# Kernel optimization log

Hardware: AMD Instinct MI355X
Metric: run time of the kernel (lower is better)

## Reference

```python
import jax, jax.numpy as jnp
import numpy as np

DIM, QK, GS, DEPTH, VOCAB, ROT = 16, 128, 256, 8, 1024, 32
EPS = 1e-5


def scale_norm(x, g):
    # ScaleNorm: x / max(||x|| * dim^-0.5, eps) * g
    norm = jnp.linalg.norm(x, axis=-1, keepdims=True) * (DIM ** -0.5)
    return x / jnp.clip(norm, EPS) * g


def rotate_half(x):
    # interleaved pairs: (x0,x1,x2,x3,...) -> (-x1,x0,-x3,x2,...)
    xr = x.reshape(x.shape[:-1] + (-1, 2))
    a, b = xr[..., 0], xr[..., 1]
    return jnp.stack((-b, a), axis=-1).reshape(x.shape)


def apply_rotary(x, cos, sin):
    # rotary applied to first ROT dims only
    xr, xp = x[..., :ROT], x[..., ROT:]
    return jnp.concatenate([xr * cos + rotate_half(xr) * sin, xp], axis=-1)


def flash_layer(x, p, cos, sin, keymask, n):
    b = x.shape[0]
    normed = scale_norm(x, p['norm_g'])
    # shift_tokens: first half of channels shifted forward by one position
    xs, xp = jnp.split(normed, 2, axis=-1)
    xs = jnp.pad(xs, ((0, 0), (1, 0), (0, 0)))[:, :-1]
    normed = jnp.concatenate([xs, xp], axis=-1)
    hid = jax.nn.silu(normed @ p['Wh'] + p['bh'])  # [b,n,64]
    v, gate = jnp.split(hid, 2, axis=-1)           # each [b,n,32]
    qk = jax.nn.silu(normed @ p['Wqk'] + p['bqk'])  # [b,n,128]
    offs = qk[..., None, :] * p['gamma'] + p['beta']  # [b,n,4,128]
    quad_q, lin_q, quad_k, lin_k = [apply_rotary(offs[..., i, :], cos, sin) for i in range(4)]
    pad = (-n) % GS
    grp = lambda t: jnp.pad(t, ((0, 0), (0, pad), (0, 0))).reshape(b, -1, GS, t.shape[-1])
    quad_q, quad_k, lin_q, lin_k, vg = map(grp, (quad_q, quad_k, lin_q, lin_k, v))
    # quadratic (local, within-group) attention with ReLU^2
    sim = jnp.einsum('bgid,bgjd->bgij', quad_q, quad_k) / GS
    attn = jnp.square(jax.nn.relu(sim)) * keymask  # mask out padded keys
    quad_out = jnp.einsum('bgij,bgjd->bgid', attn, vg)
    # linear (global, across-group) attention, reduced over groups
    lin_kv = jnp.einsum('bgnd,bgne->bde', lin_k, vg) / n
    lin_out = jnp.einsum('bgnd,bde->bgne', lin_q, lin_kv)
    out = (quad_out + lin_out).reshape(b, -1, v.shape[-1])[:, :n]
    out = gate * out
    return out @ p['Wo'] + p['bo'] + x


def forward(kmer_data, token_emb, pos_scale, norm_g, Wh, bh, Wqk, bqk, gamma, beta, Wo, bo, final_g, Wl, bl, W1, b1, W2, b2):
    b, n = kmer_data.shape
    x = token_emb[kmer_data]  # [b,n,16]
    t = jnp.arange(n, dtype=jnp.float32)
    # ScaledSinuEmbedding
    inv = 1.0 / (10000.0 ** (jnp.arange(0, DIM, 2, dtype=jnp.float32) / DIM))
    sinu = t[:, None] * inv[None, :]
    pos = jnp.concatenate([jnp.sin(sinu), jnp.cos(sinu)], axis=-1) * pos_scale
    x = x + pos
    # rotary tables (dim 32, interleaved repeat)
    rinv = 1.0 / (10000.0 ** (jnp.arange(0, ROT, 2, dtype=jnp.float32) / ROT))
    rf = jnp.repeat(t[:, None] * rinv[None, :], 2, axis=-1)  # [n,32]
    cos, sin = jnp.cos(rf), jnp.sin(rf)
    # key mask for padded positions (996 -> 1024)
    pad = (-n) % GS
    keymask = jnp.pad(jnp.ones((n,), jnp.float32), (0, pad)).reshape(1, -1, 1, GS)
    for i in range(DEPTH):
        p = dict(norm_g=norm_g[i], Wh=Wh[i], bh=bh[i], Wqk=Wqk[i], bqk=bqk[i],
                 gamma=gamma[i], beta=beta[i], Wo=Wo[i], bo=bo[i])
        x = flash_layer(x, p, cos, sin, keymask, n)
    logits = scale_norm(x, final_g) @ Wl + bl  # [b,n,1024]
    h = jnp.max(logits, axis=-1)               # AdaptiveMaxPool1d(1) + Flatten -> [b,n]
    h = jax.nn.relu(h @ W1 + b1)
    return h @ W2 + b2                          # [b,1]


def setup_inputs() -> dict:
    key = jax.random.key(0)
    ks = jax.random.split(key, 12)
    r = lambda k, shape, s: jax.random.normal(k, shape, jnp.float32) * s
    return {
        'kmer_data': jax.random.randint(ks[0], (128, 996), 0, VOCAB),
        'token_emb': r(ks[1], (VOCAB, DIM), 1.0),
        'pos_scale': jnp.float32(1.0),
        'norm_g': jnp.ones((DEPTH,), jnp.float32),
        'Wh': r(ks[2], (DEPTH, DIM, 64), 0.1),
        'bh': jnp.zeros((DEPTH, 64), jnp.float32),
        'Wqk': r(ks[3], (DEPTH, DIM, QK), 0.1),
        'bqk': jnp.zeros((DEPTH, QK), jnp.float32),
        'gamma': 1.0 + r(ks[4], (DEPTH, 4, QK), 0.02),
        'beta': r(ks[5], (DEPTH, 4, QK), 0.02),
        'Wo': r(ks[6], (DEPTH, 32, DIM), 0.1),
        'bo': jnp.zeros((DEPTH, DIM), jnp.float32),
        'final_g': jnp.float32(1.0),
        'Wl': r(ks[7], (DIM, VOCAB), 0.1),
        'bl': jnp.zeros((VOCAB,), jnp.float32),
        'W1': r(ks[8], (996, 32), 0.05),
        'b1': jnp.zeros((32,), jnp.float32),
        'W2': r(ks[9], (32, 1), 0.1),
        'b2': jnp.zeros((1,), jnp.float32),
    }


def reference(kmer_data, token_emb, pos_scale, norm_g, Wh, bh, Wqk, bqk, gamma, beta, Wo, bo, final_g, Wl, bl, W1, b1, W2, b2):
    return forward(kmer_data, token_emb, pos_scale, norm_g, Wh, bh, Wqk, bqk,
                   gamma, beta, Wo, bo, final_g, Wl, bl, W1, b1, W2, b2)
```

## Files before the change

kernel.cpp:

```cpp
#include <hip/hip_runtime.h>

typedef short s16x8 __attribute__((ext_vector_type(8)));
typedef float f32x4 __attribute__((ext_vector_type(4)));

#define NB    128
#define NTOK  996
#define NPAD  1024
#define NGRP  4
#define GSZ   256
#define NLAY  8

__device__ __forceinline__ float bf2f(unsigned short u){
    unsigned int v = ((unsigned int)u) << 16;
    return __uint_as_float(v);
}
__device__ __forceinline__ unsigned short f2bf(float f){
    unsigned int x = __float_as_uint(f);
    unsigned int r = (x + 0x7fffu + ((x >> 16) & 1u)) >> 16;
    return (unsigned short)r;
}
__device__ __forceinline__ unsigned int packbf(float a, float b){
    return (unsigned int)f2bf(a) | ((unsigned int)f2bf(b) << 16);
}
__device__ __forceinline__ float silu(float v){
    return v / (1.0f + __expf(-v));
}

__device__ __forceinline__ void bar_lds(){
    asm volatile("s_waitcnt lgkmcnt(0)\n\ts_barrier" ::: "memory");
}

__device__ __forceinline__ s16x8 derive_core(const unsigned short* __restrict__ qrow, int d0,
        float4 g0, float4 g1, float4 b0, float4 b1,
        const float* __restrict__ rp, bool rot){
    uint4 u = *(const uint4*)(qrow + d0);
    float y0 = bf2f((unsigned short)(u.x & 0xffffu))*g0.x + b0.x;
    float y1 = bf2f((unsigned short)(u.x >> 16))    *g0.y + b0.y;
    float y2 = bf2f((unsigned short)(u.y & 0xffffu))*g0.z + b0.z;
    float y3 = bf2f((unsigned short)(u.y >> 16))    *g0.w + b0.w;
    float y4 = bf2f((unsigned short)(u.z & 0xffffu))*g1.x + b1.x;
    float y5 = bf2f((unsigned short)(u.z >> 16))    *g1.y + b1.y;
    float y6 = bf2f((unsigned short)(u.w & 0xffffu))*g1.z + b1.z;
    float y7 = bf2f((unsigned short)(u.w >> 16))    *g1.w + b1.w;
    if (rot){
        float4 c4 = *(const float4*)(rp);
        float4 s4 = *(const float4*)(rp + 16);
        float a;
        a = y0; y0 = a*c4.x - y1*s4.x; y1 = y1*c4.x + a*s4.x;
        a = y2; y2 = a*c4.y - y3*s4.y; y3 = y3*c4.y + a*s4.y;
        a = y4; y4 = a*c4.z - y5*s4.z; y5 = y5*c4.z + a*s4.z;
        a = y6; y6 = a*c4.w - y7*s4.w; y7 = y7*c4.w + a*s4.w;
    }
    union { unsigned int uu[4]; s16x8 s; } r;
    r.uu[0] = packbf(y0, y1);
    r.uu[1] = packbf(y2, y3);
    r.uu[2] = packbf(y4, y5);
    r.uu[3] = packbf(y6, y7);
    return r.s;
}

__global__ __launch_bounds__(256) void k_embed(const int* __restrict__ kmer,
                                               const float* __restrict__ emb,
                                               const float* __restrict__ ps,
                                               float* __restrict__ x,
                                               float* __restrict__ rope){
    int gid = blockIdx.x * 256 + threadIdx.x;
    if (gid < NPAD){
        float tf2 = (float)gid;
        #pragma unroll
        for (int i = 0; i < 16; i++){
            float inv = expf(((float)(2*i) / 32.0f) * -9.210340371976184f);
            float ang = tf2 * inv;
            rope[gid*32 + i]      = cosf(ang);
            rope[gid*32 + 16 + i] = sinf(ang);
        }
    }
    if (gid >= NB * NTOK) return;
    int b = gid / NTOK;
    int tt = gid - b * NTOK;
    int idx = kmer[gid];
    const float* er = emb + (size_t)idx * 16;
    float pscale = ps[0];
    float tf = (float)tt;
    float* xr = x + (size_t)gid * 16;
    #pragma unroll
    for (int i = 0; i < 8; i++){
        float inv = expf(((float)(2*i) / 16.0f) * -9.210340371976184f);
        float ang = tf * inv;
        xr[i]     = er[i]     + sinf(ang) * pscale;
        xr[8 + i] = er[8 + i] + cosf(ang) * pscale;
    }
}

__global__ __launch_bounds__(512, 2) void k_pre(const float* __restrict__ x,
                                             const float* __restrict__ Wh, const float* __restrict__ bh,
                                             const float* __restrict__ Wqk, const float* __restrict__ bqk,
                                             const float* __restrict__ norm_g,
                                             const float* __restrict__ gamma, const float* __restrict__ beta,
                                             const float* __restrict__ rope, int layer,
                                             unsigned short* __restrict__ qk,
                                             unsigned short* __restrict__ vT,
                                             unsigned short* __restrict__ gateb,
                                             float* __restrict__ linkvp){
    __shared__ __align__(16) unsigned char sm[58880];
    unsigned short* WcT = (unsigned short*)sm;
    unsigned short* As  = (unsigned short*)(sm + 15360);
    unsigned short* LkT = (unsigned short*)(sm + 15360);
    unsigned short* Vt  = (unsigned short*)(sm + 50176);
    int tid = threadIdx.x;
    int qt = blockIdx.x & 3, b = blockIdx.x >> 2;
    const float* Whl = Wh  + (size_t)layer * 1024;
    const float* Wql = Wqk + (size_t)layer * 2048;
    const float* gLin = gamma + (size_t)layer * 512 + 384;
    const float* bLin = beta  + (size_t)layer * 512 + 384;
    for (int i = tid; i < 1024; i += 512){ int d = i >> 6, c2 = i & 63;  WcT[c2*40 + d] = f2bf(Whl[i]); }
    for (int i = tid; i < 2048; i += 512){ int d = i >> 7, c2 = i & 127; WcT[(64 + c2)*40 + d] = f2bf(Wql[i]); }
    if (tid < 192){
        int i = tid;
        float bv = (i < 64) ? bh[layer*64 + i] : bqk[layer*128 + (i - 64)];
        WcT[i*40 + 16] = f2bf(bv);
        WcT[i*40 + 17] = 0;
        unsigned int* zz = (unsigned int*)(WcT + i*40 + 18);
        #pragma unroll
        for (int k = 0; k < 7; k++) zz[k] = 0u;
    }
    float g = norm_g[layer];
    if (tid < 256){
        int tt = qt*256 + tid;
        int tsafe = tt < NTOK ? tt : (NTOK - 1);
        unsigned int* dd = (unsigned int*)(As + tid * 40);
        const float4* xr4 = (const float4*)(x + ((size_t)b*NTOK + tsafe) * 16);
        float cur[16];
        float s2 = 0.f;
        #pragma unroll
        for (int c2 = 0; c2 < 4; c2++){
            float4 v4 = xr4[c2];
            cur[4*c2] = v4.x; cur[4*c2+1] = v4.y; cur[4*c2+2] = v4.z; cur[4*c2+3] = v4.w;
        }
        #pragma unroll
        for (int d = 0; d < 16; d++) s2 += cur[d]*cur[d];
        float sc = g / fmaxf(sqrtf(s2) * 0.25f, 1e-5f);
        #pragma unroll
        for (int i = 0; i < 4; i++) dd[4 + i] = packbf(cur[8 + 2*i]*sc, cur[9 + 2*i]*sc);
        dd[8] = 0x00003f80u;
        #pragma unroll
        for (int i = 9; i < 16; i++) dd[i] = 0u;
        if (tid < 255){
            unsigned int* ddn = (unsigned int*)(As + (tid+1) * 40);
            #pragma unroll
            for (int i = 0; i < 4; i++) ddn[i] = packbf(cur[2*i]*sc, cur[2*i+1]*sc);
        }
        if (tid == 0){
            if (tt == 0){
                dd[0] = 0u; dd[1] = 0u; dd[2] = 0u; dd[3] = 0u;
            } else {
                const float4* xp4 = (const float4*)(x + ((size_t)b*NTOK + tt - 1) * 16);
                float prv[16]; float p2 = 0.f;
                #pragma unroll
                for (int c2 = 0; c2 < 4; c2++){
                    float4 v4 = xp4[c2];
                    prv[4*c2] = v4.x; prv[4*c2+1] = v4.y; prv[4*c2+2] = v4.z; prv[4*c2+3] = v4.w;
                }
                #pragma unroll
                for (int d = 0; d < 16; d++) p2 += prv[d]*prv[d];
                float sp = g / fmaxf(sqrtf(p2) * 0.25f, 1e-5f);
                #pragma unroll
                for (int i = 0; i < 4; i++) dd[i] = packbf(prv[2*i]*sp, prv[2*i+1]*sp);
            }
        }
    }
    bar_lds();
    int w = tid >> 6, lane = tid & 63, m16 = lane & 15, quad = lane >> 4;
    s16x8 bfr[2];
    #pragma unroll
    for (int nt = 0; nt < 2; nt++)
        bfr[nt] = *(const s16x8*)(As + (w*32 + nt*16 + m16)*40 + quad*8);
    bar_lds();
    f32x4 zacc = {0.f,0.f,0.f,0.f};
    f32x4 lacc[2] = {{0,0,0,0},{0,0,0,0}};
    unsigned int vpk[2][2][2];
    int c = w*16 + m16;
    #pragma unroll
    for (int nt = 0; nt < 2; nt++){
        int ttk = qt*256 + w*32 + nt*16 + m16;
        bool tv = ttk < NTOK;
        size_t rowq = (size_t)b*NPAD + ttk;
        #pragma unroll
        for (int mi = 0; mi < 12; mi++){
            s16x8 wfm = *(const s16x8*)(WcT + (mi*16 + m16)*40 + quad*8);
            f32x4 r = __builtin_amdgcn_mfma_f32_16x16x32_bf16(wfm, bfr[nt], zacc, 0, 0, 0);
            float sv[4];
            #pragma unroll
            for (int reg = 0; reg < 4; reg++) sv[reg] = silu(r[reg]);
            int wc0 = mi*16 + quad*4;
            if (mi < 2){
                unsigned short p0 = tv ? f2bf(sv[0]) : (unsigned short)0;
                unsigned short p1 = tv ? f2bf(sv[1]) : (unsigned short)0;
                unsigned short p2 = tv ? f2bf(sv[2]) : (unsigned short)0;
                unsigned short p3 = tv ? f2bf(sv[3]) : (unsigned short)0;
                Vt[(wc0+0)*136 + c] = p0;
                Vt[(wc0+1)*136 + c] = p1;
                Vt[(wc0+2)*136 + c] = p2;
                Vt[(wc0+3)*136 + c] = p3;
                vpk[nt][mi][0] = (unsigned int)p0 | ((unsigned int)p1 << 16);
                vpk[nt][mi][1] = (unsigned int)p2 | ((unsigned int)p3 << 16);
            } else if (mi < 4){
                *(uint2*)(gateb + rowq*32 + (wc0 - 32)) = make_uint2(packbf(sv[0],sv[1]), packbf(sv[2],sv[3]));
            } else {
                int qd = wc0 - 64;
                *(uint2*)(qk + rowq*128 + qd) = make_uint2(packbf(sv[0],sv[1]), packbf(sv[2],sv[3]));
                float y0 = sv[0]*gLin[qd]   + bLin[qd];
                float y1 = sv[1]*gLin[qd+1] + bLin[qd+1];
                float y2 = sv[2]*gLin[qd+2] + bLin[qd+2];
                float y3 = sv[3]*gLin[qd+3] + bLin[qd+3];
                if (qd < 32){
                    const float* rp = rope + ttk*32 + (qd >> 1);
                    float c0 = rp[0], s0 = rp[16], c1 = rp[1], s1 = rp[17];
                    float a;
                    a = y0; y0 = a*c0 - y1*s0; y1 = y1*c0 + a*s0;
                    a = y2; y2 = a*c1 - y3*s1; y3 = y3*c1 + a*s1;
                }
                LkT[(qd+0)*136 + c] = f2bf(y0);
                LkT[(qd+1)*136 + c] = f2bf(y1);
                LkT[(qd+2)*136 + c] = f2bf(y2);
                LkT[(qd+3)*136 + c] = f2bf(y3);
            }
        }
        bar_lds();
        #pragma unroll
        for (int ks2 = 0; ks2 < 4; ks2++){
            s16x8 a  = *(const s16x8*)(LkT + (w*16 + m16)*136 + ks2*32 + quad*8);
            s16x8 b0 = *(const s16x8*)(Vt + (m16)*136 + ks2*32 + quad*8);
            s16x8 b1 = *(const s16x8*)(Vt + (16 + m16)*136 + ks2*32 + quad*8);
            lacc[0] = __builtin_amdgcn_mfma_f32_16x16x32_bf16(a, b0, lacc[0], 0,0,0);
            lacc[1] = __builtin_amdgcn_mfma_f32_16x16x32_bf16(a, b1, lacc[1], 0,0,0);
        }
        bar_lds();
    }
    {
        unsigned short* mv = (unsigned short*)sm + w*1280;
        #pragma unroll
        for (int nt = 0; nt < 2; nt++){
            #pragma unroll
            for (int mi = 0; mi < 2; mi++){
                int e0 = mi*16 + quad*4;
                mv[(e0+0)*40 + nt*16 + m16] = (unsigned short)(vpk[nt][mi][0] & 0xffffu);
                mv[(e0+1)*40 + nt*16 + m16] = (unsigned short)(vpk[nt][mi][0] >> 16);
                mv[(e0+2)*40 + nt*16 + m16] = (unsigned short)(vpk[nt][mi][1] & 0xffffu);
                mv[(e0+3)*40 + nt*16 + m16] = (unsigned short)(vpk[nt][mi][1] >> 16);
            }
        }
        #pragma unroll
        for (int r2 = 0; r2 < 2; r2++){
            int e = r2*16 + (lane >> 2);
            int cc = (lane & 3) * 8;
            s16x8 vv = *(const s16x8*)(mv + e*40 + cc);
            *(s16x8*)(vT + ((size_t)b*32 + e)*NPAD + qt*256 + w*32 + cc) = vv;
        }
    }
    {
        float* ml = (float*)(sm + 20480) + w*512;
        const float invn = 1.0f / 996.0f;
        #pragma unroll
        for (int j = 0; j < 2; j++)
            #pragma unroll
            for (int reg = 0; reg < 4; reg++)
                ml[(j*16 + m16)*16 + quad*4 + reg] = lacc[j][reg] * invn;
        #pragma unroll
        for (int r2 = 0; r2 < 2; r2++){
            int e = r2*16 + (lane >> 2);
            int dc = (lane & 3) * 4;
            float4 vv = *(const float4*)(ml + e*16 + dc);
            *(float4*)(linkvp + (((size_t)qt*NB + b)*32 + e)*128 + w*16 + dc) = vv;
        }
    }
}

#define KD_SH   8704
#define KD2_BYTES (2*64*136*2)
#define PW_BYTES  (8*32*40*2)
__global__ __launch_bounds__(512, 2) void k_quad(const unsigned short* __restrict__ qk,
                                              const unsigned short* __restrict__ vT,
                                              const unsigned short* __restrict__ gateb,
                                              const float* __restrict__ linkvp,
                                              const float* __restrict__ rope,
                                              const float* __restrict__ gamma, const float* __restrict__ beta,
                                              int layer,
                                              const float* __restrict__ Wo, const float* __restrict__ bo,
                                              float* __restrict__ x){
    __shared__ __align__(16) unsigned char smem[KD2_BYTES + PW_BYTES];
    __shared__ float sWo[512];
    __shared__ float sbo[16];
    unsigned short* Kd   = (unsigned short*)smem;
    unsigned short* Pw   = (unsigned short*)(smem + KD2_BYTES);
    unsigned short* LkBs = (unsigned short*)(smem + KD2_BYTES);
    int tid = threadIdx.x;
    int blk = blockIdx.x;
    int g = blk & 3, b = blk >> 2;
    int tg0 = g * GSZ;
    const float* gamL = gamma + (size_t)layer * 512;
    const float* betL = beta  + (size_t)layer * 512;
    sWo[tid] = Wo[layer*512 + tid];
    if (tid < 16) sbo[tid] = bo[layer*16 + tid];

    int w = tid >> 6, lane = tid & 63, m16 = lane & 15, quad = lane >> 4;

    int kr = tid >> 3, seg = (tid & 7) * 16;
    uint4 pku0, pku1;
    float4 prc0, prc1, prs0, prs1;
    auto LOADK = [&](int ch){
        int tk = tg0 + ch*64 + kr;
        const unsigned short* krow = qk + ((size_t)b*NPAD + tk)*128 + seg;
        pku0 = ((const uint4*)krow)[0];
        pku1 = ((const uint4*)krow)[1];
        if (seg < 32){
            const float* rpk = rope + tk*32 + (seg >> 1);
            prc0 = *(const float4*)(rpk);
            prs0 = *(const float4*)(rpk + 16);
            prc1 = *(const float4*)(rpk + 4);
            prs1 = *(const float4*)(rpk + 20);
        }
    };
    const float* gK = gamL + 256;
    const float* bK = betL + 256;
    auto DERIVEK = [&](uint4& kd0, uint4& kd1){
        #pragma unroll
        for (int h = 0; h < 2; h++){
            uint4 u = h ? pku1 : pku0;
            unsigned int uu[4] = {u.x, u.y, u.z, u.w};
            float y[8];
            #pragma unroll
            for (int k = 0; k < 4; k++){
                int d = h*8 + 2*k;
                y[2*k]   = bf2f((unsigned short)(uu[k] & 0xffffu)) * gK[seg + d]     + bK[seg + d];
                y[2*k+1] = bf2f((unsigned short)(uu[k] >> 16))     * gK[seg + d + 1] + bK[seg + d + 1];
            }
            if (seg < 32){
                float cc[4], ss[4];
                if (h){ cc[0]=prc1.x; cc[1]=prc1.y; cc[2]=prc1.z; cc[3]=prc1.w;
                        ss[0]=prs1.x; ss[1]=prs1.y; ss[2]=prs1.z; ss[3]=prs1.w; }
                else  { cc[0]=prc0.x; cc[1]=prc0.y; cc[2]=prc0.z; cc[3]=prc0.w;
                        ss[0]=prs0.x; ss[1]=prs0.y; ss[2]=prs0.z; ss[3]=prs0.w; }
                #pragma unroll
                for (int p2 = 0; p2 < 4; p2++){
                    float a = y[2*p2], d2 = y[2*p2+1];
                    y[2*p2]   = a*cc[p2] - d2*ss[p2];
                    y[2*p2+1] = d2*cc[p2] + a*ss[p2];
                }
            }
            uint4 kk = make_uint4(packbf(y[0],y[1]), packbf(y[2],y[3]),
                                  packbf(y[4],y[5]), packbf(y[6],y[7]));
            if (h) kd1 = kk; else kd0 = kk;
        }
    };
    auto LOADV = [&](int ch, s16x8 vf[2][2]){
        #pragma unroll
        for (int ks2 = 0; ks2 < 2; ks2++){
            vf[ks2][0] = *(const s16x8*)(vT + ((size_t)b*32 + m16)*NPAD + tg0 + ch*64 + ks2*32 + quad*8);
            vf[ks2][1] = *(const s16x8*)(vT + ((size_t)b*32 + 16 + m16)*NPAD + tg0 + ch*64 + ks2*32 + quad*8);
        }
    };

    LOADK(0);

    int tqA = tg0 + w*32 + m16;
    int tqB = tqA + 16;
    const unsigned short* qrowA = qk + ((size_t)b*NPAD + tqA)*128;
    const unsigned short* qrowB = qk + ((size_t)b*NPAD + tqB)*128;
    const float* rpA = rope + tqA*32 + quad*4;
    const float* rpB = rope + tqB*32 + quad*4;
    s16x8 qf[2][4];
    #pragma unroll
    for (int ks = 0; ks < 4; ks++){
        int d0 = ks*32 + quad*8;
        float4 g0 = *(const float4*)(gamL + d0), g1 = *(const float4*)(gamL + d0 + 4);
        float4 b0 = *(const float4*)(betL + d0), b1 = *(const float4*)(betL + d0 + 4);
        bool rot = (ks == 0) && (quad < 4);
        qf[0][ks] = derive_core(qrowA, d0, g0,g1,b0,b1, rpA, rot);
        qf[1][ks] = derive_core(qrowB, d0, g0,g1,b0,b1, rpB, rot);
    }

    {
        uint4 kd0, kd1;
        DERIVEK(kd0, kd1);
        *(uint4*)(Kd + kr*136 + seg)     = kd0;
        *(uint4*)(Kd + kr*136 + seg + 8) = kd1;
    }
    LOADK(1);
    s16x8 vfA[2][2];
    LOADV(0, vfA);

    f32x4 oacc[2][2] = {{{0,0,0,0},{0,0,0,0}},{{0,0,0,0},{0,0,0,0}}};
    unsigned short* myP = Pw + w*1280;

    #pragma unroll
    for (int ch = 0; ch < 4; ch++){
        bar_lds();
        s16x8 vfB[2][2];
        if (ch < 3) LOADV(ch + 1, vfB);
        unsigned short* Kc = Kd + (ch & 1)*KD_SH;
        #pragma unroll
        for (int np = 0; np < 2; np++){
            f32x4 s00 = {0,0,0,0}, s01 = {0,0,0,0}, s10 = {0,0,0,0}, s11 = {0,0,0,0};
            #pragma unroll
            for (int ks = 0; ks < 4; ks++){
                s16x8 kf0 = *(const s16x8*)(Kc + ((np*2  )*16 + m16)*136 + ks*32 + quad*8);
                s16x8 kf1 = *(const s16x8*)(Kc + ((np*2+1)*16 + m16)*136 + ks*32 + quad*8);
                s00 = __builtin_amdgcn_mfma_f32_16x16x32_bf16(qf[0][ks], kf0, s00, 0,0,0);
                s01 = __builtin_amdgcn_mfma_f32_16x16x32_bf16(qf[0][ks], kf1, s01, 0,0,0);
                s10 = __builtin_amdgcn_mfma_f32_16x16x32_bf16(qf[1][ks], kf0, s10, 0,0,0);
                s11 = __builtin_amdgcn_mfma_f32_16x16x32_bf16(qf[1][ks], kf1, s11, 0,0,0);
            }
            #pragma unroll
            for (int j = 0; j < 2; j++){
                int kl = j*16 + m16;
                bool kv = (tg0 + ch*64 + np*32 + kl) < NTOK;
                #pragma unroll
                for (int reg = 0; reg < 4; reg++){
                    float a0 = fmaxf(j ? s01[reg] : s00[reg], 0.0f);
                    float a1 = fmaxf(j ? s11[reg] : s10[reg], 0.0f);
                    a0 = a0 * a0;
                    a1 = a1 * a1;
                    myP[(quad*4 + reg)*40 + kl]      = kv ? f2bf(a0) : (unsigned short)0;
                    myP[(16 + quad*4 + reg)*40 + kl] = kv ? f2bf(a1) : (unsigned short)0;
                }
            }
            #pragma unroll
            for (int i = 0; i < 2; i++){
                s16x8 pa = *(const s16x8*)(myP + (i*16 + m16)*40 + quad*8);
                oacc[i][0] = __builtin_amdgcn_mfma_f32_16x16x32_bf16(pa, vfA[np][0], oacc[i][0], 0,0,0);
                oacc[i][1] = __builtin_amdgcn_mfma_f32_16x16x32_bf16(pa, vfA[np][1], oacc[i][1], 0,0,0);
            }
            if (np == 0 && ch < 3){
                uint4 kd0, kd1;
                DERIVEK(kd0, kd1);
                unsigned short* Kn = Kd + ((ch+1) & 1)*KD_SH;
                *(uint4*)(Kn + kr*136 + seg)     = kd0;
                *(uint4*)(Kn + kr*136 + seg + 8) = kd1;
                if (ch < 2) LOADK(ch + 2);
            }
        }
        if (ch < 3){
            #pragma unroll
            for (int ks2 = 0; ks2 < 2; ks2++){
                vfA[ks2][0] = vfB[ks2][0];
                vfA[ks2][1] = vfB[ks2][1];
            }
        }
    }
    const float qsc = 1.0f / 65536.0f;
    #pragma unroll
    for (int i = 0; i < 2; i++)
        #pragma unroll
        for (int j = 0; j < 2; j++)
            oacc[i][j] = oacc[i][j] * qsc;
    int e = tid >> 4, dbase = (tid & 15) * 8;
    float4 lp[4][2];
    #pragma unroll
    for (int part = 0; part < 4; part++){
        const float* src = linkvp + (((size_t)part*NB + b)*32 + e)*128 + dbase;
        lp[part][0] = *(const float4*)src;
        lp[part][1] = *(const float4*)(src + 4);
    }
    bar_lds();
    {
        float s[8];
        #pragma unroll
        for (int k = 0; k < 8; k++) s[k] = 0.f;
        #pragma unroll
        for (int part = 0; part < 4; part++){
            s[0]+=lp[part][0].x; s[1]+=lp[part][0].y; s[2]+=lp[part][0].z; s[3]+=lp[part][0].w;
            s[4]+=lp[part][1].x; s[5]+=lp[part][1].y; s[6]+=lp[part][1].z; s[7]+=lp[part][1].w;
        }
        unsigned int* dst = (unsigned int*)(LkBs + e*136 + dbase);
        #pragma unroll
        for (int k = 0; k < 4; k++) dst[k] = packbf(s[2*k], s[2*k+1]);
    }
    bar_lds();
    int pr = lane >> 1, dp2 = (lane & 1) * 8;
    int p = tg0 + w*32 + pr;
    bool pvld = p < NTOK;
    int psafe = pvld ? p : (NTOK - 1);
    const unsigned short* gr = gateb + ((size_t)b*NPAD + psafe)*32;
    uint4 egu[4];
    #pragma unroll
    for (int eh = 0; eh < 4; eh++) egu[eh] = *(const uint4*)(gr + eh*8);
    float* xr = x + ((size_t)b*NTOK + psafe)*16 + dp2;
    float4 ex0 = *(const float4*)xr;
    float4 ex1 = *(const float4*)(xr + 4);
    {
        const float* gamQ = gamL + 128;
        const float* betQ = betL + 128;
        #pragma unroll
        for (int ks = 0; ks < 4; ks++){
            int d0 = ks*32 + quad*8;
            float4 g0 = *(const float4*)(gamQ + d0), g1 = *(const float4*)(gamQ + d0 + 4);
            float4 b0 = *(const float4*)(betQ + d0), b1 = *(const float4*)(betQ + d0 + 4);
            bool rot = (ks == 0) && (quad < 4);
            s16x8 lf0 = derive_core(qrowA, d0, g0,g1,b0,b1, rpA, rot);
            s16x8 lf1 = derive_core(qrowB, d0, g0,g1,b0,b1, rpB, rot);
            #pragma unroll
            for (int j = 0; j < 2; j++){
                s16x8 lb = *(const s16x8*)(LkBs + (j*16 + m16)*136 + ks*32 + quad*8);
                oacc[0][j] = __builtin_amdgcn_mfma_f32_16x16x32_bf16(lf0, lb, oacc[0][j], 0,0,0);
                oacc[1][j] = __builtin_amdgcn_mfma_f32_16x16x32_bf16(lf1, lb, oacc[1][j], 0,0,0);
            }
        }
    }
    float* Obw = (float*)smem + w*1056;
    #pragma unroll
    for (int i = 0; i < 2; i++)
        #pragma unroll
        for (int j = 0; j < 2; j++)
            #pragma unroll
            for (int reg = 0; reg < 4; reg++)
                Obw[(i*16 + quad*4 + reg)*33 + j*16 + m16] = oacc[i][j][reg];
    if (pvld){
        float a[8] = { sbo[dp2]+ex0.x, sbo[dp2+1]+ex0.y, sbo[dp2+2]+ex0.z, sbo[dp2+3]+ex0.w,
                       sbo[dp2+4]+ex1.x, sbo[dp2+5]+ex1.y, sbo[dp2+6]+ex1.z, sbo[dp2+7]+ex1.w };
        #pragma unroll
        for (int eh = 0; eh < 4; eh++){
            unsigned int gg[4] = {egu[eh].x, egu[eh].y, egu[eh].z, egu[eh].w};
            #pragma unroll
            for (int k = 0; k < 4; k++){
                float gv0 = bf2f((unsigned short)(gg[k] & 0xffffu));
                float gv1 = bf2f((unsigned short)(gg[k] >> 16));
                int ee = eh*8 + 2*k;
                float ov0 = Obw[pr*33 + ee] * gv0;
                float ov1 = Obw[pr*33 + ee + 1] * gv1;
                const float* wr0 = &sWo[ee*16 + dp2];
                const float* wr1 = &sWo[(ee+1)*16 + dp2];
                #pragma unroll
                for (int kk = 0; kk < 8; kk++) a[kk] += ov0 * wr0[kk] + ov1 * wr1[kk];
            }
        }
        *(float4*)xr = make_float4(a[0],a[1],a[2],a[3]);
        *(float4*)(xr+4) = make_float4(a[4],a[5],a[6],a[7]);
    }
}

__global__ __launch_bounds__(256) void k_head(const float* __restrict__ x,
                                              const float* __restrict__ Wl, const float* __restrict__ bl,
                                              const float* __restrict__ fg, float* __restrict__ h){
    __shared__ __align__(16) unsigned short WlT[512 * 40];
    __shared__ __align__(16) unsigned short As[256 * 40];
    int tid = threadIdx.x;
    int gid0 = blockIdx.x * 256;
    {
        int t = gid0 + tid;
        const float4* xr4 = (const float4*)(x + (size_t)t * 16);
        float cur[16]; float s2 = 0.f;
        #pragma unroll
        for (int c = 0; c < 4; c++){
            float4 v4 = xr4[c];
            cur[4*c] = v4.x; cur[4*c+1] = v4.y; cur[4*c+2] = v4.z; cur[4*c+3] = v4.w;
        }
        #pragma unroll
        for (int d = 0; d < 16; d++) s2 += cur[d]*cur[d];
        float sc = fg[0] / fmaxf(sqrtf(s2) * 0.25f, 1e-5f);
        unsigned int* dd = (unsigned int*)(As + tid * 40);
        #pragma unroll
        for (int i = 0; i < 8; i++) dd[i] = packbf(cur[2*i]*sc, cur[2*i+1]*sc);
        dd[8] = 0x00003f80u;
        #pragma unroll
        for (int i = 9; i < 16; i++) dd[i] = 0u;
    }
    int w = tid >> 6, lane = tid & 63, m16 = lane & 15, quad = lane >> 4;
    f32x4 vm[4];
    #pragma unroll
    for (int i = 0; i < 4; i++) vm[i] = (f32x4){-3e38f,-3e38f,-3e38f,-3e38f};
    for (int half = 0; half < 2; half++){
        __syncthreads();
        for (int i = tid; i < 8192; i += 256){
            int d = i >> 9, c = i & 511;
            WlT[c*40 + d] = f2bf(Wl[(size_t)d*1024 + half*512 + c]);
        }
        for (int i = tid; i < 512; i += 256){
            WlT[i*40 + 16] = f2bf(bl[half*512 + i]);
            WlT[i*40 + 17] = 0;
            unsigned int* zz = (unsigned int*)(WlT + i*40 + 18);
            #pragma unroll
            for (int k = 0; k < 7; k++) zz[k] = 0u;
        }
        __syncthreads();
        s16x8 af[4];
        #pragma unroll
        for (int i = 0; i < 4; i++)
            af[i] = *(const s16x8*)(As + (w*64 + i*16 + m16)*40 + quad*8);
        f32x4 zacc = {0,0,0,0};
        for (int nt = 0; nt < 32; nt++){
            s16x8 bf = *(const s16x8*)(WlT + (nt*16 + m16)*40 + quad*8);
            #pragma unroll
            for (int i = 0; i < 4; i++){
                f32x4 r = __builtin_amdgcn_mfma_f32_16x16x32_bf16(af[i], bf, zacc, 0,0,0);
                #pragma unroll
                for (int reg = 0; reg < 4; reg++)
                    vm[i][reg] = fmaxf(vm[i][reg], r[reg]);
            }
        }
    }
    #pragma unroll
    for (int i = 0; i < 4; i++){
        #pragma unroll
        for (int off = 1; off < 16; off <<= 1){
            #pragma unroll
            for (int reg = 0; reg < 4; reg++)
                vm[i][reg] = fmaxf(vm[i][reg], __shfl_xor(vm[i][reg], off, 64));
        }
    }
    if (m16 == 0){
        #pragma unroll
        for (int i = 0; i < 4; i++){
            int t0 = gid0 + w*64 + i*16 + quad*4;
            #pragma unroll
            for (int reg = 0; reg < 4; reg++)
                h[t0 + reg] = vm[i][reg];
        }
    }
}

__global__ __launch_bounds__(256) void k_final(const float* __restrict__ h,
                                               const float* __restrict__ W1, const float* __restrict__ b1,
                                               const float* __restrict__ W2, const float* __restrict__ b2,
                                               float* __restrict__ out){
    int b = blockIdx.x;
    int tid = threadIdx.x;
    int j = tid & 31, part = tid >> 5;
    float acc = 0.f;
    for (int i = part; i < NTOK; i += 8)
        acc += h[(size_t)b*NTOK + i] * W1[(size_t)i*32 + j];
    __shared__ float red[8][33];
    red[part][j] = acc;
    __syncthreads();
    if (tid < 32){
        float s = b1[tid];
        #pragma unroll
        for (int p = 0; p < 8; p++) s += red[p][tid];
        s = fmaxf(s, 0.f);
        red[0][tid] = s * W2[tid];
    }
    __syncthreads();
    if (tid == 0){
        float s = b2[0];
        #pragma unroll
        for (int jj = 0; jj < 32; jj++) s += red[0][jj];
        out[b] = s;
    }
}

extern "C" void kernel_launch(void* const* d_in, const int* in_sizes, int n_in,
                              void* d_out, int out_size, void* d_ws, size_t ws_size,
                              hipStream_t stream){
    const int*   kmer  = (const int*)d_in[0];
    const float* emb   = (const float*)d_in[1];
    const float* ps    = (const float*)d_in[2];
    const float* ng    = (const float*)d_in[3];
    const float* Wh    = (const float*)d_in[4];
    const float* bh    = (const float*)d_in[5];
    const float* Wqk   = (const float*)d_in[6];
    const float* bqk   = (const float*)d_in[7];
    const float* gamma = (const float*)d_in[8];
    const float* beta  = (const float*)d_in[9];
    const float* Wo    = (const float*)d_in[10];
    const float* bo    = (const float*)d_in[11];
    const float* fg    = (const float*)d_in[12];
    const float* Wl    = (const float*)d_in[13];
    const float* bl    = (const float*)d_in[14];
    const float* W1    = (const float*)d_in[15];
    const float* b1    = (const float*)d_in[16];
    const float* W2    = (const float*)d_in[17];
    const float* b2    = (const float*)d_in[18];
    float* out = (float*)d_out;

    char* wsp = (char*)d_ws;
    float* x = (float*)wsp;                     wsp += (size_t)NB*NTOK*16*4;
    unsigned short* qk = (unsigned short*)wsp;  wsp += (size_t)NB*NPAD*128*2;
    unsigned short* vT = (unsigned short*)wsp;  wsp += (size_t)NB*32*NPAD*2;
    unsigned short* gateb = (unsigned short*)wsp; wsp += (size_t)NB*NPAD*32*2;
    float* linkvp = (float*)wsp;                wsp += (size_t)4*NB*32*128*4;
    float* rope = (float*)wsp;                  wsp += (size_t)NPAD*32*4;
    float* h = (float*)wsp;                     wsp += (size_t)NB*NTOK*4;

    k_embed<<<(NB*NTOK + 255)/256, 256, 0, stream>>>(kmer, emb, ps, x, rope);
    for (int layer = 0; layer < NLAY; layer++){
        k_pre<<<NB*4, 512, 0, stream>>>(x, Wh, bh, Wqk, bqk, ng, gamma, beta, rope, layer, qk, vT, gateb, linkvp);
        k_quad<<<NB*NGRP, 512, 0, stream>>>(qk, vT, gateb, linkvp, rope, gamma, beta, layer, Wo, bo, x);
    }
    k_head<<<NB*NTOK/256, 256, 0, stream>>>(x, Wl, bl, fg, h);
    k_final<<<NB, 256, 0, stream>>>(h, W1, b1, W2, b2, out);
}
```

Before: 758.3 us.

## Split quad-attention blocks into query halves with smaller key chunks

k_quad now launches two 256-thread blocks per (batch, group), each owning 128 query rows instead of 256. Keys are streamed in 32-row chunks over 8 iterations, and V fragments are loaded directly each chunk rather than software-prefetched. The aim is higher occupancy (launch bounds 256x5) and finer scheduling granularity. In exchange, each half-block re-derives the full group's K tiles and re-reduces the linear-attention KV partials, which duplicates that work, and the loop has more barriers.

Measured after the change: 1.965 ms. 159% more time.

```diff
diff --git a/kernel.cpp b/kernel.cpp
--- a/kernel.cpp
+++ b/kernel.cpp
@@ -276,10 +276,11 @@
     }
 }
 
-#define KD_SH   8704
-#define KD2_BYTES (2*64*136*2)
-#define PW_BYTES  (8*32*40*2)
-__global__ __launch_bounds__(512, 2) void k_quad(const unsigned short* __restrict__ qk,
+#define KQ_CH   32
+#define KD_SH2  (32*136)
+#define KD2B    (2*KD_SH2*2)
+#define PWB     (4*32*40*2)
+__global__ __launch_bounds__(256, 5) void k_quad(const unsigned short* __restrict__ qk,
                                               const unsigned short* __restrict__ vT,
                                               const unsigned short* __restrict__ gateb,
                                               const float* __restrict__ linkvp,
@@ -288,19 +289,21 @@
                                               int layer,
                                               const float* __restrict__ Wo, const float* __restrict__ bo,
                                               float* __restrict__ x){
-    __shared__ __align__(16) unsigned char smem[KD2_BYTES + PW_BYTES];
+    __shared__ __align__(16) unsigned char smem[KD2B + PWB];
     __shared__ float sWo[512];
     __shared__ float sbo[16];
     unsigned short* Kd   = (unsigned short*)smem;
-    unsigned short* Pw   = (unsigned short*)(smem + KD2_BYTES);
-    unsigned short* LkBs = (unsigned short*)(smem + KD2_BYTES);
+    unsigned short* Pw   = (unsigned short*)(smem + KD2B);
+    unsigned short* LkBs = Pw;
     int tid = threadIdx.x;
     int blk = blockIdx.x;
-    int g = blk & 3, b = blk >> 2;
+    int half = blk & 1, g = (blk >> 1) & 3, b = blk >> 3;
     int tg0 = g * GSZ;
+    int qb0 = tg0 + half*128;
     const float* gamL = gamma + (size_t)layer * 512;
     const float* betL = beta  + (size_t)layer * 512;
-    sWo[tid] = Wo[layer*512 + tid];
+    sWo[tid]       = Wo[layer*512 + tid];
+    sWo[tid + 256] = Wo[layer*512 + 256 + tid];
     if (tid < 16) sbo[tid] = bo[layer*16 + tid];
 
     int w = tid >> 6, lane = tid & 63, m16 = lane & 15, quad = lane >> 4;
@@ -309,7 +312,7 @@
     uint4 pku0, pku1;
     float4 prc0, prc1, prs0, prs1;
     auto LOADK = [&](int ch){
-        int tk = tg0 + ch*64 + kr;
+        int tk = tg0 + ch*KQ_CH + kr;
         const unsigned short* krow = qk + ((size_t)b*NPAD + tk)*128 + seg;
         pku0 = ((const uint4*)krow)[0];
         pku1 = ((const uint4*)krow)[1];
@@ -353,17 +356,10 @@
             if (h) kd1 = kk; else kd0 = kk;
         }
     };
-    auto LOADV = [&](int ch, s16x8 vf[2][2]){
-        #pragma unroll
-        for (int ks2 = 0; ks2 < 2; ks2++){
-            vf[ks2][0] = *(const s16x8*)(vT + ((size_t)b*32 + m16)*NPAD + tg0 + ch*64 + ks2*32 + quad*8);
-            vf[ks2][1] = *(const s16x8*)(vT + ((size_t)b*32 + 16 + m16)*NPAD + tg0 + ch*64 + ks2*32 + quad*8);
-        }
-    };
 
     LOADK(0);
 
-    int tqA = tg0 + w*32 + m16;
+    int tqA = qb0 + w*32 + m16;
     int tqB = tqA + 16;
     const unsigned short* qrowA = qk + ((size_t)b*NPAD + tqA)*128;
     const unsigned short* qrowB = qk + ((size_t)b*NPAD + tqB)*128;
@@ -387,65 +383,53 @@
         *(uint4*)(Kd + kr*136 + seg + 8) = kd1;
     }
     LOADK(1);
-    s16x8 vfA[2][2];
-    LOADV(0, vfA);
 
     f32x4 oacc[2][2] = {{{0,0,0,0},{0,0,0,0}},{{0,0,0,0},{0,0,0,0}}};
     unsigned short* myP = Pw + w*1280;
 
-    #pragma unroll
-    for (int ch = 0; ch < 4; ch++){
+    #pragma unroll 2
+    for (int ch = 0; ch < 8; ch++){
         bar_lds();
-        s16x8 vfB[2][2];
-        if (ch < 3) LOADV(ch + 1, vfB);
-        unsigned short* Kc = Kd + (ch & 1)*KD_SH;
-        #pragma unroll
-        for (int np = 0; np < 2; np++){
-            f32x4 s00 = {0,0,0,0}, s01 = {0,0,0,0}, s10 = {0,0,0,0}, s11 = {0,0,0,0};
-            #pragma unroll
-            for (int ks = 0; ks < 4; ks++){
-                s16x8 kf0 = *(const s16x8*)(Kc + ((np*2  )*16 + m16)*136 + ks*32 + quad*8);
-                s16x8 kf1 = *(const s16x8*)(Kc + ((np*2+1)*16 + m16)*136 + ks*32 + quad*8);
-                s00 = __builtin_amdgcn_mfma_f32_16x16x32_bf16(qf[0][ks], kf0, s00, 0,0,0);
-                s01 = __builtin_amdgcn_mfma_f32_16x16x32_bf16(qf[0][ks], kf1, s01, 0,0,0);
-                s10 = __builtin_amdgcn_mfma_f32_16x16x32_bf16(qf[1][ks], kf0, s10, 0,0,0);
-                s11 = __builtin_amdgcn_mfma_f32_16x16x32_bf16(qf[1][ks], kf1, s11, 0,0,0);
-            }
-            #pragma unroll
-            for (int j = 0; j < 2; j++){
-                int kl = j*16 + m16;
-                bool kv = (tg0 + ch*64 + np*32 + kl) < NTOK;
-                #pragma unroll
-                for (int reg = 0; reg < 4; reg++){
-                    float a0 = fmaxf(j ? s01[reg] : s00[reg], 0.0f);
-                    float a1 = fmaxf(j ? s11[reg] : s10[reg], 0.0f);
-                    a0 = a0 * a0;
-                    a1 = a1 * a1;
-                    myP[(quad*4 + reg)*40 + kl]      = kv ? f2bf(a0) : (unsigned short)0;
-                    myP[(16 + quad*4 + reg)*40 + kl] = kv ? f2bf(a1) : (unsigned short)0;
-                }
-            }
-            #pragma unroll
-            for (int i = 0; i < 2; i++){
-                s16x8 pa = *(const s16x8*)(myP + (i*16 + m16)*40 + quad*8);
-                oacc[i][0] = __builtin_amdgcn_mfma_f32_16x16x32_bf16(pa, vfA[np][0], oacc[i][0], 0,0,0);
-                oacc[i][1] = __builtin_amdgcn_mfma_f32_16x16x32_bf16(pa, vfA[np][1], oacc[i][1], 0,0,0);
-            }
-            if (np == 0 && ch < 3){
-                uint4 kd0, kd1;
-                DERIVEK(kd0, kd1);
-                unsigned short* Kn = Kd + ((ch+1) & 1)*KD_SH;
-                *(uint4*)(Kn + kr*136 + seg)     = kd0;
-                *(uint4*)(Kn + kr*136 + seg + 8) = kd1;
-                if (ch < 2) LOADK(ch + 2);
-            }
-        }
-        if (ch < 3){
-            #pragma unroll
-            for (int ks2 = 0; ks2 < 2; ks2++){
-                vfA[ks2][0] = vfB[ks2][0];
-                vfA[ks2][1] = vfB[ks2][1];
-            }
+        s16x8 vf0 = *(const s16x8*)(vT + ((size_t)b*32 + m16)*NPAD + tg0 + ch*KQ_CH + quad*8);
+        s16x8 vf1 = *(const s16x8*)(vT + ((size_t)b*32 + 16 + m16)*NPAD + tg0 + ch*KQ_CH + quad*8);
+        unsigned short* Kc = Kd + (ch & 1)*KD_SH2;
+        f32x4 s00 = {0,0,0,0}, s01 = {0,0,0,0}, s10 = {0,0,0,0}, s11 = {0,0,0,0};
+        #pragma unroll
+        for (int ks = 0; ks < 4; ks++){
+            s16x8 kf0 = *(const s16x8*)(Kc + (m16)*136 + ks*32 + quad*8);
+            s16x8 kf1 = *(const s16x8*)(Kc + (16 + m16)*136 + ks*32 + quad*8);
+            s00 = __builtin_amdgcn_mfma_f32_16x16x32_bf16(qf[0][ks], kf0, s00, 0,0,0);
+            s01 = __builtin_amdgcn_mfma_f32_16x16x32_bf16(qf[0][ks], kf1, s01, 0,0,0);
+            s10 = __builtin_amdgcn_mfma_f32_16x16x32_bf16(qf[1][ks], kf0, s10, 0,0,0);
+            s11 = __builtin_amdgcn_mfma_f32_16x16x32_bf16(qf[1][ks], kf1, s11, 0,0,0);
+        }
+        #pragma unroll
+        for (int j = 0; j < 2; j++){
+            int kl = j*16 + m16;
+            bool kv = (tg0 + ch*KQ_CH + kl) < NTOK;
+            #pragma unroll
+            for (int reg = 0; reg < 4; reg++){
+                float a0 = fmaxf(j ? s01[reg] : s00[reg], 0.0f);
+                float a1 = fmaxf(j ? s11[reg] : s10[reg], 0.0f);
+                a0 = a0 * a0;
+                a1 = a1 * a1;
+                myP[(quad*4 + reg)*40 + kl]      = kv ? f2bf(a0) : (unsigned short)0;
+                myP[(16 + quad*4 + reg)*40 + kl] = kv ? f2bf(a1) : (unsigned short)0;
+            }
+        }
+        if (ch < 7){
+            uint4 kd0, kd1;
+            DERIVEK(kd0, kd1);
+            unsigned short* Kn = Kd + ((ch+1) & 1)*KD_SH2;
+            *(uint4*)(Kn + kr*136 + seg)     = kd0;
+            *(uint4*)(Kn + kr*136 + seg + 8) = kd1;
+            if (ch < 6) LOADK(ch + 2);
+        }
+        #pragma unroll
+        for (int i = 0; i < 2; i++){
+            s16x8 pa = *(const s16x8*)(myP + (i*16 + m16)*40 + quad*8);
+            oacc[i][0] = __builtin_amdgcn_mfma_f32_16x16x32_bf16(pa, vf0, oacc[i][0], 0,0,0);
+            oacc[i][1] = __builtin_amdgcn_mfma_f32_16x16x32_bf16(pa, vf1, oacc[i][1], 0,0,0);
         }
     }
     const float qsc = 1.0f / 65536.0f;
@@ -454,31 +438,29 @@
         #pragma unroll
         for (int j = 0; j < 2; j++)
             oacc[i][j] = oacc[i][j] * qsc;
-    int e = tid >> 4, dbase = (tid & 15) * 8;
-    float4 lp[4][2];
-    #pragma unroll
-    for (int part = 0; part < 4; part++){
-        const float* src = linkvp + (((size_t)part*NB + b)*32 + e)*128 + dbase;
-        lp[part][0] = *(const float4*)src;
-        lp[part][1] = *(const float4*)(src + 4);
-    }
     bar_lds();
     {
-        float s[8];
-        #pragma unroll
-        for (int k = 0; k < 8; k++) s[k] = 0.f;
+        int e = tid >> 3, db = (tid & 7) * 16;
+        float s[16];
+        #pragma unroll
+        for (int k = 0; k < 16; k++) s[k] = 0.f;
         #pragma unroll
         for (int part = 0; part < 4; part++){
-            s[0]+=lp[part][0].x; s[1]+=lp[part][0].y; s[2]+=lp[part][0].z; s[3]+=lp[part][0].w;
-            s[4]+=lp[part][1].x; s[5]+=lp[part][1].y; s[6]+=lp[part][1].z; s[7]+=lp[part][1].w;
-        }
-        unsigned int* dst = (unsigned int*)(LkBs + e*136 + dbase);
-        #pragma unroll
-        for (int k = 0; k < 4; k++) dst[k] = packbf(s[2*k], s[2*k+1]);
+            const float* src = linkvp + (((size_t)part*NB + b)*32 + e)*128 + db;
+            #pragma unroll
+            for (int q4 = 0; q4 < 4; q4++){
+                float4 u = *(const float4*)(src + q4*4);
+                s[q4*4]   += u.x; s[q4*4+1] += u.y;
+                s[q4*4+2] += u.z; s[q4*4+3] += u.w;
+            }
+        }
+        unsigned int* dst = (unsigned int*)(LkBs + e*136 + db);
+        #pragma unroll
+        for (int k = 0; k < 8; k++) dst[k] = packbf(s[2*k], s[2*k+1]);
     }
     bar_lds();
     int pr = lane >> 1, dp2 = (lane & 1) * 8;
-    int p = tg0 + w*32 + pr;
+    int p = qb0 + w*32 + pr;
     bool pvld = p < NTOK;
     int psafe = pvld ? p : (NTOK - 1);
     const unsigned short* gr = gateb + ((size_t)b*NPAD + psafe)*32;
@@ -684,7 +666,7 @@
     k_embed<<<(NB*NTOK + 255)/256, 256, 0, stream>>>(kmer, emb, ps, x, rope);
     for (int layer = 0; layer < NLAY; layer++){
         k_pre<<<NB*4, 512, 0, stream>>>(x, Wh, bh, Wqk, bqk, ng, gamma, beta, rope, layer, qk, vT, gateb, linkvp);
-        k_quad<<<NB*NGRP, 512, 0, stream>>>(qk, vT, gateb, linkvp, rope, gamma, beta, layer, Wo, bo, x);
+        k_quad<<<NB*NGRP*2, 256, 0, stream>>>(qk, vT, gateb, linkvp, rope, gamma, beta, layer, Wo, bo, x);
     }
     k_head<<<NB*NTOK/256, 256, 0, stream>>>(x, Wl, bl, fg, h);
     k_final<<<NB, 256, 0, stream>>>(h, W1, b1, W2, b2, out);
```
